# Performance work log

Measured on AMD Instinct MI355X. Metric: run time of the kernel, lower is better.

## Reference

```python
import jax, jax.numpy as jnp
import numpy as np

VOCAB, NUM_LABELS, EMB, H = 50000, 5, 512, 1024
B, S = 32, 256


def setup_inputs() -> dict:
    key = jax.random.key(0)
    ks = jax.random.split(key, 7)
    tokens = jax.random.randint(ks[0], (B, S), 0, VOCAB)
    scale_e = 0.05
    emb = jax.random.normal(ks[1], (VOCAB, EMB), dtype=jnp.float32) * scale_e
    # Keras LSTM kernels: input kernel [EMB,4H], recurrent kernel [H,4H], bias [4H]
    W = jax.random.normal(ks[2], (EMB, 4 * H), dtype=jnp.float32) / np.sqrt(EMB)
    U = jax.random.normal(ks[3], (H, 4 * H), dtype=jnp.float32) / np.sqrt(H)
    # unit_forget_bias=True: forget-gate bias block initialized to 1
    b = jnp.concatenate([
        jnp.zeros((H,), jnp.float32),
        jnp.ones((H,), jnp.float32),
        jnp.zeros((2 * H,), jnp.float32),
    ])
    Wd = jax.random.normal(ks[4], (H, NUM_LABELS), dtype=jnp.float32) / np.sqrt(H)
    bd = jnp.zeros((NUM_LABELS,), jnp.float32)
    return {"tokens": tokens, "emb": emb, "W": W, "U": U, "b": b, "Wd": Wd, "bd": bd}


def _lstm_last_h(x, W, U, b):
    # x: [B,S,EMB] -> last hidden state [B,H]
    xt = jnp.swapaxes(x, 0, 1)  # [S,B,EMB]
    # precompute input projections for all steps: [S,B,4H]
    xz = jnp.einsum('sbe,eg->sbg', xt, W) + b
    h0 = jnp.zeros((x.shape[0], H), x.dtype)
    c0 = jnp.zeros((x.shape[0], H), x.dtype)

    def step(carry, xz_t):
        h, c = carry
        z = xz_t + h @ U  # [B,4H]
        i, f, g, o = jnp.split(z, 4, axis=-1)  # Keras gate order i,f,c,o
        i = jax.nn.sigmoid(i)
        f = jax.nn.sigmoid(f)
        g = jnp.tanh(g)
        o = jax.nn.sigmoid(o)
        c = f * c + i * g
        h = o * jnp.tanh(c)
        return (h, c), None

    (h_last, _), _ = jax.lax.scan(step, (h0, c0), xz)
    return h_last


def reference(tokens, emb, W, U, b, Wd, bd):
    x = emb[tokens]  # [B,S,EMB] embedding lookup
    h = _lstm_last_h(x, W, U, b)  # [B,H]
    logits = h @ Wd + bd  # [B,NUM_LABELS]
    return logits
```

## Files before the change

kernel.cpp:

```cpp
#include <hip/hip_runtime.h>
#include <hip/hip_fp16.h>

#define B_   32
#define S_   256
#define EMB_ 512
#define H_   1024
#define G4_  4096
#define NL_  5
#define NBLK 128

typedef _Float16 f16x8 __attribute__((ext_vector_type(8)));
typedef float f32x4 __attribute__((ext_vector_type(4)));
typedef unsigned long long ull;

__device__ inline ull ldq(const ull* p) {
  return __hip_atomic_load(p, __ATOMIC_RELAXED, __HIP_MEMORY_SCOPE_AGENT);
}
__device__ inline unsigned ldw(const unsigned* p) {
  return __hip_atomic_load(p, __ATOMIC_RELAXED, __HIP_MEMORY_SCOPE_AGENT);
}
__device__ inline void stw(unsigned* p, unsigned v) {
  __hip_atomic_store(p, v, __ATOMIC_RELAXED, __HIP_MEMORY_SCOPE_AGENT);
}

__global__ __launch_bounds__(256) void k_transposeK(const float* __restrict__ src,
                                                    float* __restrict__ dst, int K) {
  __shared__ float tile[32][33];
  int c0 = blockIdx.x * 32, k0 = blockIdx.y * 32;
  int tx = threadIdx.x & 31, ty = threadIdx.x >> 5;
#pragma unroll
  for (int i = 0; i < 4; ++i)
    tile[ty + 8 * i][tx] = src[(size_t)(k0 + ty + 8 * i) * G4_ + c0 + tx];
  __syncthreads();
#pragma unroll
  for (int i = 0; i < 4; ++i)
    dst[(size_t)(c0 + ty + 8 * i) * K + k0 + tx] = tile[tx][ty + 8 * i];
}

__global__ __launch_bounds__(256) void k_prepU16(const float* __restrict__ Ut,
                                                 f16x8* __restrict__ Ubf) {
  int gid = blockIdx.x * 256 + threadIdx.x;
  int l = gid & 63;
  int bxws = gid >> 6;
  int n = l & 15, kgrp = l >> 4;
  int s = bxws & 7, bw = bxws >> 3;
  int w = bw & 3, bx = bw >> 2;
  int g = n & 3, ju = n >> 2;
  int gcol = g * 1024 + bx * 4 + ju;
  int kbase = w * 256 + s * 32 + kgrp * 8;
  const float4* f = (const float4*)(Ut + (size_t)gcol * H_ + kbase);
  float4 f0 = f[0], f1 = f[1];
  float v[8] = {f0.x, f0.y, f0.z, f0.w, f1.x, f1.y, f1.z, f1.w};
  f16x8 vh, vl;
#pragma unroll
  for (int j = 0; j < 8; ++j) {
    _Float16 hi = (_Float16)v[j];
    vh[j] = hi;
    vl[j] = (_Float16)((v[j] - (float)hi) * 1024.f);
  }
  Ubf[(size_t)bxws * 128 + l] = vh;
  Ubf[(size_t)bxws * 128 + 64 + l] = vl;
}

__global__ __launch_bounds__(256) void k_prepW16(const float* __restrict__ Wt,
                                                 unsigned short* __restrict__ Wf16) {
  int gid = blockIdx.x * 256 + threadIdx.x;
  int l = gid & 63, fi = gid >> 6;
  int kc = fi & 15, ug = fi >> 4;
  int n16 = l & 15, kgrp = l >> 4;
  int gcol = (n16 & 3) * 1024 + ug * 4 + (n16 >> 2);
  const float4* f = (const float4*)(Wt + (size_t)gcol * 512 + kc * 32 + kgrp * 8);
  float4 f0 = f[0], f1 = f[1];
  float v[8] = {f0.x, f0.y, f0.z, f0.w, f1.x, f1.y, f1.z, f1.w};
  union { unsigned short u[8]; uint4 q; } o;
#pragma unroll
  for (int j = 0; j < 8; ++j) o.u[j] = __half_as_ushort(__float2half_rn(v[j]));
  *(uint4*)(Wf16 + ((size_t)fi * 64 + l) * 8) = o.q;
}

__global__ __launch_bounds__(256) void k_prepX(const int* __restrict__ tokens,
                                               const float* __restrict__ emb,
                                               unsigned short* __restrict__ Xf16) {
  int gid = blockIdx.x * 256 + threadIdx.x;
  int seg = gid & 63, row = gid >> 6;
  int s = row >> 5, b = row & 31;
  int tok = tokens[b * 256 + s];
  const float4* f = (const float4*)(emb + (size_t)tok * EMB_ + seg * 8);
  float4 f0 = f[0], f1 = f[1];
  float v[8] = {f0.x, f0.y, f0.z, f0.w, f1.x, f1.y, f1.z, f1.w};
  union { unsigned short u[8]; uint4 q; } o;
#pragma unroll
  for (int j = 0; j < 8; ++j) o.u[j] = __half_as_ushort(__float2half_rn(v[j]));
  *(uint4*)(Xf16 + (size_t)row * 512 + seg * 8) = o.q;
}

__global__ __launch_bounds__(512, 2) void k_steps11(
    const f16x8* __restrict__ Ubf,
    const unsigned short* __restrict__ Wf16,
    const unsigned short* __restrict__ Xf16,
    const float* __restrict__ bias,
    unsigned* __restrict__ T0, unsigned* __restrict__ T1,
    unsigned* __restrict__ flg) {
  __shared__ f16x8 UL[8192];
  __shared__ float red[4096];

  const int tid = threadIdx.x;
  const int bx = blockIdx.x;
  const int l = tid & 63, w = tid >> 6;

#pragma unroll
  for (int i = 0; i < 16; ++i) {
    int flat = i * 512 + tid;
    int ll = flat & 63, s8 = (flat >> 6) & 7, ks = (flat >> 9) & 3;
    int pl = (flat >> 11) & 1, cg = flat >> 12;
    size_t fi = (size_t)((bx * 2 + cg) * 4 + ks) * 8 + s8;
    UL[flat] = Ubf[fi * 128 + pl * 64 + ll];
  }

  const int gb = tid & 31, gu = tid >> 5;
  const int gm2 = gb >> 4, gcg = gu >> 2, gju = gu & 3;
  const int gle = ((gb & 15) >> 2) * 16 + gju * 4;
  const int grr = gb & 3;
  const int widx = (((gb >> 4) * 128 + bx) * 16 + (gb & 15)) * 4 + (gu >> 1);
  float bia[4];
#pragma unroll
  for (int g = 0; g < 4; ++g) bia[g] = bias[g * 1024 + bx * 8 + gu];
  float creg = 0.f;

  const int ks_w = w >> 1;
  const int xrow0 = (l & 15) * 512 + (l >> 4) * 8;
  const unsigned* myflg = flg + (size_t)((w * 16 + (l >> 2)) * 4 + (l & 3)) * 16;

  __syncthreads();

  for (int t = 0; t < S_; ++t) {
    const ull* R64 = (const ull*)((t & 1) ? T0 : T1);
    unsigned* WrT = (t & 1) ? T1 : T0;

    f32x4 acc[2][2], accL[2][2];
#pragma unroll
    for (int cg = 0; cg < 2; ++cg)
#pragma unroll
      for (int m2 = 0; m2 < 2; ++m2) {
        acc[cg][m2] = (f32x4){0.f, 0.f, 0.f, 0.f};
        accL[cg][m2] = (f32x4){0.f, 0.f, 0.f, 0.f};
      }
    {
      const unsigned short* Xt = Xf16 + (size_t)t * 16384;
#pragma unroll
      for (int c2 = 0; c2 < 2; ++c2) {
        int kc = w * 2 + c2;
        f16x8 xa0 = *(const f16x8*)(Xt + xrow0 + kc * 32);
        f16x8 xa1 = *(const f16x8*)(Xt + 8192 + xrow0 + kc * 32);
        f16x8 wb0 = *(const f16x8*)(Wf16 + ((size_t)((bx * 2 + 0) * 16 + kc) * 64 + l) * 8);
        f16x8 wb1 = *(const f16x8*)(Wf16 + ((size_t)((bx * 2 + 1) * 16 + kc) * 64 + l) * 8);
        acc[0][0] = __builtin_amdgcn_mfma_f32_16x16x32_f16(xa0, wb0, acc[0][0], 0, 0, 0);
        acc[0][1] = __builtin_amdgcn_mfma_f32_16x16x32_f16(xa1, wb0, acc[0][1], 0, 0, 0);
        acc[1][0] = __builtin_amdgcn_mfma_f32_16x16x32_f16(xa0, wb1, acc[1][0], 0, 0, 0);
        acc[1][1] = __builtin_amdgcn_mfma_f32_16x16x32_f16(xa1, wb1, acc[1][1], 0, 0, 0);
      }
    }

    if (t > 0) {
      const unsigned tg = (unsigned)t;
      while (true) {
        unsigned v = ldw(myflg);
        if (__all((int)(v >= tg))) break;
        __builtin_amdgcn_s_sleep(1);
      }
      union F { ull q[2]; f16x8 v; };
      F A[2][4];
#pragma unroll
      for (int m2 = 0; m2 < 2; ++m2)
#pragma unroll
        for (int s = 0; s < 4; ++s) {
          int kidx = w * 16 + s * 4 + (l >> 4);
          int b64 = ((m2 * 128 + kidx) * 16 + (l & 15)) * 2;
          A[m2][s].q[0] = ldq(R64 + b64);
          A[m2][s].q[1] = ldq(R64 + b64 + 1);
        }
#pragma unroll
      for (int s = 0; s < 4; ++s) {
        int s8 = (w & 1) * 4 + s;
#pragma unroll
        for (int cg = 0; cg < 2; ++cg) {
          f16x8 uhf = UL[cg * 4096 + ks_w * 512 + s8 * 64 + l];
          f16x8 ulf = UL[cg * 4096 + 2048 + ks_w * 512 + s8 * 64 + l];
          acc[cg][0]  = __builtin_amdgcn_mfma_f32_16x16x32_f16(A[0][s].v, uhf, acc[cg][0], 0, 0, 0);
          acc[cg][1]  = __builtin_amdgcn_mfma_f32_16x16x32_f16(A[1][s].v, uhf, acc[cg][1], 0, 0, 0);
          accL[cg][0] = __builtin_amdgcn_mfma_f32_16x16x32_f16(A[0][s].v, ulf, accL[cg][0], 0, 0, 0);
          accL[cg][1] = __builtin_amdgcn_mfma_f32_16x16x32_f16(A[1][s].v, ulf, accL[cg][1], 0, 0, 0);
        }
      }
    }

#pragma unroll
    for (int cg = 0; cg < 2; ++cg)
#pragma unroll
      for (int m2 = 0; m2 < 2; ++m2)
        acc[cg][m2] += accL[cg][m2] * 9.765625e-4f;

    if (w < 4) {
#pragma unroll
      for (int cg = 0; cg < 2; ++cg) {
        *(f32x4*)(&red[((w * 2 + 0) * 2 + cg) * 256 + l * 4]) = acc[cg][0];
        *(f32x4*)(&red[((w * 2 + 1) * 2 + cg) * 256 + l * 4]) = acc[cg][1];
      }
    }
    __syncthreads();
    if (w >= 4) {
      int w4 = w - 4;
#pragma unroll
      for (int cg = 0; cg < 2; ++cg) {
        f32x4* p0 = (f32x4*)(&red[((w4 * 2 + 0) * 2 + cg) * 256 + l * 4]);
        f32x4* p1 = (f32x4*)(&red[((w4 * 2 + 1) * 2 + cg) * 256 + l * 4]);
        *p0 += acc[cg][0];
        *p1 += acc[cg][1];
      }
    }
    __syncthreads();

    if (tid < 256) {
      float z[4];
#pragma unroll
      for (int g = 0; g < 4; ++g) z[g] = bia[g];
#pragma unroll
      for (int w4 = 0; w4 < 4; ++w4) {
        int sb = ((w4 * 2 + gm2) * 2 + gcg) * 256;
#pragma unroll
        for (int g = 0; g < 4; ++g)
          z[g] += red[sb + (gle + g) * 4 + grr];
      }
      float ig = 1.f / (1.f + __expf(-z[0]));
      float fg = 1.f / (1.f + __expf(-z[1]));
      float gg = tanhf(z[2]);
      float og = 1.f / (1.f + __expf(-z[3]));
      creg = fg * creg + ig * gg;
      float hv = og * tanhf(creg);
      unsigned pk = (unsigned)__half_as_ushort(__float2half_rn(hv));
      unsigned other = (unsigned)__shfl_xor((int)pk, 32, 64);
      if ((gu & 1) == 0)
        stw(WrT + widx, (pk & 0xffffu) | (other << 16));
      asm volatile("s_waitcnt vmcnt(0)" ::: "memory");
      if ((tid & 63) == 0)
        stw(flg + (size_t)(bx * 4 + (tid >> 6)) * 16, (unsigned)(t + 1));
    }
    __syncthreads();
  }
}

__global__ __launch_bounds__(256) void k_head6(const unsigned* __restrict__ T,
                                               const float* __restrict__ Wd,
                                               const float* __restrict__ bd,
                                               float* __restrict__ out) {
  __shared__ float red[32 * 9];
  int lbl = blockIdx.x;
  int tid = threadIdx.x;
  int b = tid >> 3, ks = tid & 7;
  float acc = 0.f;
  for (int k = ks * 128; k < ks * 128 + 128; ++k) {
    int idx = (((b >> 4) * 128 + (k >> 3)) * 16 + (b & 15)) * 4 + ((k & 7) >> 1);
    unsigned wv = T[idx];
    unsigned short h16 = (unsigned short)((k & 1) ? (wv >> 16) : (wv & 0xffffu));
    acc += __half2float(__ushort_as_half(h16)) * Wd[k * NL_ + lbl];
  }
  red[b * 9 + ks] = acc;
  __syncthreads();
  if (tid < 32) {
    float s = bd[lbl];
#pragma unroll
    for (int i = 0; i < 8; ++i) s += red[tid * 9 + i];
    out[tid * NL_ + lbl] = s;
  }
}

extern "C" void kernel_launch(void* const* d_in, const int* in_sizes, int n_in,
                              void* d_out, int out_size, void* d_ws, size_t ws_size,
                              hipStream_t stream) {
  const int* tokens  = (const int*)d_in[0];
  const float* emb   = (const float*)d_in[1];
  const float* W     = (const float*)d_in[2];
  const float* U     = (const float*)d_in[3];
  const float* bias  = (const float*)d_in[4];
  const float* Wd    = (const float*)d_in[5];
  const float* bd    = (const float*)d_in[6];
  float* out = (float*)d_out;

  char* ws = (char*)d_ws;
  unsigned short* Xf16 = (unsigned short*)ws;
  unsigned short* Wf16 = (unsigned short*)(ws + 8388608);
  float* Ut          = (float*)(ws + 16777216);
  float* Wt          = (float*)(ws + 33554432);
  f16x8* Ubf         = (f16x8*)(ws + 41943040);
  unsigned* T0       = (unsigned*)(ws + 58720256);
  unsigned* T1       = (unsigned*)(ws + 58785792);
  unsigned* flg      = (unsigned*)(ws + 58851328);

  hipMemsetAsync(flg, 0, 32768, stream);
  k_transposeK<<<dim3(128, 32), 256, 0, stream>>>(U, Ut, 1024);
  k_prepU16<<<2048, 256, 0, stream>>>(Ut, Ubf);
  k_transposeK<<<dim3(128, 16), 256, 0, stream>>>(W, Wt, 512);
  k_prepW16<<<1024, 256, 0, stream>>>(Wt, Wf16);
  k_prepX<<<2048, 256, 0, stream>>>(tokens, emb, Xf16);

  k_steps11<<<NBLK, 512, 0, stream>>>(Ubf, Wf16, Xf16, bias, T0, T1, flg);

  k_head6<<<NL_, 256, 0, stream>>>(T1, Wd, bd, out);
}
```

Baseline: 1.139 ms.

## Double-buffer gate reduction, drop a barrier, stream low U half from global

Restructures the per-step reduction in the persistent LSTM kernel. All 8 waves now write partials into a double-buffered LDS array and all 512 threads reduce them into a gate buffer, which removes one of the three barriers per step. The low-precision half of U is re-read from global/L2 each step instead of living in LDS, halving the U footprint in shared memory. Sigmoid and tanh are replaced with fast rcp/exp forms, which costs some accuracy and risks overflow in the exp-based tanh for large inputs.

```diff
diff --git a/kernel.cpp b/kernel.cpp
--- a/kernel.cpp
+++ b/kernel.cpp
@@ -21,6 +21,13 @@
 }
 __device__ inline void stw(unsigned* p, unsigned v) {
   __hip_atomic_store(p, v, __ATOMIC_RELAXED, __HIP_MEMORY_SCOPE_AGENT);
+}
+__device__ inline float sigm(float x) {
+  return __builtin_amdgcn_rcpf(1.f + __expf(-x));
+}
+__device__ inline float ftanh(float x) {
+  float e = __expf(2.f * x);
+  return (e - 1.f) * __builtin_amdgcn_rcpf(e + 1.f);
 }
 
 __global__ __launch_bounds__(256) void k_transposeK(const float* __restrict__ src,
@@ -94,37 +101,42 @@
   *(uint4*)(Xf16 + (size_t)row * 512 + seg * 8) = o.q;
 }
 
-__global__ __launch_bounds__(512, 2) void k_steps11(
+__global__ __launch_bounds__(512, 2) void k_steps12(
     const f16x8* __restrict__ Ubf,
     const unsigned short* __restrict__ Wf16,
     const unsigned short* __restrict__ Xf16,
     const float* __restrict__ bias,
     unsigned* __restrict__ T0, unsigned* __restrict__ T1,
     unsigned* __restrict__ flg) {
-  __shared__ f16x8 UL[8192];
-  __shared__ float red[4096];
+  __shared__ f16x8 UL[4096];
+  __shared__ float red[2][8192];
+  __shared__ float zg[2][1056];
+  __shared__ float bias_s[32];
 
   const int tid = threadIdx.x;
   const int bx = blockIdx.x;
   const int l = tid & 63, w = tid >> 6;
 
 #pragma unroll
-  for (int i = 0; i < 16; ++i) {
+  for (int i = 0; i < 8; ++i) {
     int flat = i * 512 + tid;
     int ll = flat & 63, s8 = (flat >> 6) & 7, ks = (flat >> 9) & 3;
-    int pl = (flat >> 11) & 1, cg = flat >> 12;
+    int cg = flat >> 11;
     size_t fi = (size_t)((bx * 2 + cg) * 4 + ks) * 8 + s8;
-    UL[flat] = Ubf[fi * 128 + pl * 64 + ll];
-  }
+    UL[flat] = Ubf[fi * 128 + ll];
+  }
+  if (tid < 32) {
+    int cg = tid >> 4, n16 = tid & 15;
+    bias_s[tid] = bias[(n16 & 3) * 1024 + (bx * 2 + cg) * 4 + (n16 >> 2)];
+  }
+
+  const int e = tid & 255, m = tid >> 8;
+  const int n16r = (e >> 2) & 15;
+  const int zb = m * 16 + (e >> 6) * 4 + (e & 3);
 
   const int gb = tid & 31, gu = tid >> 5;
-  const int gm2 = gb >> 4, gcg = gu >> 2, gju = gu & 3;
-  const int gle = ((gb & 15) >> 2) * 16 + gju * 4;
-  const int grr = gb & 3;
   const int widx = (((gb >> 4) * 128 + bx) * 16 + (gb & 15)) * 4 + (gu >> 1);
-  float bia[4];
-#pragma unroll
-  for (int g = 0; g < 4; ++g) bia[g] = bias[g * 1024 + bx * 8 + gu];
+  const int zrd = gb * 33 + (gu >> 2) * 16 + (gu & 3) * 4;
   float creg = 0.f;
 
   const int ks_w = w >> 1;
@@ -134,8 +146,17 @@
   __syncthreads();
 
   for (int t = 0; t < S_; ++t) {
-    const ull* R64 = (const ull*)((t & 1) ? T0 : T1);
-    unsigned* WrT = (t & 1) ? T1 : T0;
+    const int par = t & 1;
+    const ull* R64 = (const ull*)(par ? T0 : T1);
+    unsigned* WrT = par ? T1 : T0;
+
+    f16x8 ulo[4][2];
+#pragma unroll
+    for (int s = 0; s < 4; ++s)
+#pragma unroll
+      for (int cg = 0; cg < 2; ++cg)
+        ulo[s][cg] = Ubf[((size_t)((bx * 2 + cg) * 4 + ks_w) * 8 +
+                          (w & 1) * 4 + s) * 128 + 64 + l];
 
     f32x4 acc[2][2], accL[2][2];
 #pragma unroll
@@ -184,12 +205,11 @@
         int s8 = (w & 1) * 4 + s;
 #pragma unroll
         for (int cg = 0; cg < 2; ++cg) {
-          f16x8 uhf = UL[cg * 4096 + ks_w * 512 + s8 * 64 + l];
-          f16x8 ulf = UL[cg * 4096 + 2048 + ks_w * 512 + s8 * 64 + l];
+          f16x8 uhf = UL[cg * 2048 + ks_w * 512 + s8 * 64 + l];
           acc[cg][0]  = __builtin_amdgcn_mfma_f32_16x16x32_f16(A[0][s].v, uhf, acc[cg][0], 0, 0, 0);
           acc[cg][1]  = __builtin_amdgcn_mfma_f32_16x16x32_f16(A[1][s].v, uhf, acc[cg][1], 0, 0, 0);
-          accL[cg][0] = __builtin_amdgcn_mfma_f32_16x16x32_f16(A[0][s].v, ulf, accL[cg][0], 0, 0, 0);
-          accL[cg][1] = __builtin_amdgcn_mfma_f32_16x16x32_f16(A[1][s].v, ulf, accL[cg][1], 0, 0, 0);
+          accL[cg][0] = __builtin_amdgcn_mfma_f32_16x16x32_f16(A[0][s].v, ulo[s][cg], accL[cg][0], 0, 0, 0);
+          accL[cg][1] = __builtin_amdgcn_mfma_f32_16x16x32_f16(A[1][s].v, ulo[s][cg], accL[cg][1], 0, 0, 0);
         }
       }
     }
@@ -200,43 +220,36 @@
       for (int m2 = 0; m2 < 2; ++m2)
         acc[cg][m2] += accL[cg][m2] * 9.765625e-4f;
 
-    if (w < 4) {
-#pragma unroll
-      for (int cg = 0; cg < 2; ++cg) {
-        *(f32x4*)(&red[((w * 2 + 0) * 2 + cg) * 256 + l * 4]) = acc[cg][0];
-        *(f32x4*)(&red[((w * 2 + 1) * 2 + cg) * 256 + l * 4]) = acc[cg][1];
-      }
+#pragma unroll
+    for (int cg = 0; cg < 2; ++cg)
+#pragma unroll
+      for (int m2 = 0; m2 < 2; ++m2)
+        *(f32x4*)(&red[par][(w * 4 + m2 * 2 + cg) * 256 + l * 4]) = acc[cg][m2];
+    __syncthreads();
+
+    {
+      float z0 = bias_s[n16r], z1 = bias_s[16 + n16r];
+#pragma unroll
+      for (int ww = 0; ww < 8; ++ww) {
+        z0 += red[par][(ww * 4 + m * 2 + 0) * 256 + e];
+        z1 += red[par][(ww * 4 + m * 2 + 1) * 256 + e];
+      }
+      zg[par][zb * 33 + n16r] = z0;
+      zg[par][zb * 33 + 16 + n16r] = z1;
     }
     __syncthreads();
-    if (w >= 4) {
-      int w4 = w - 4;
-#pragma unroll
-      for (int cg = 0; cg < 2; ++cg) {
-        f32x4* p0 = (f32x4*)(&red[((w4 * 2 + 0) * 2 + cg) * 256 + l * 4]);
-        f32x4* p1 = (f32x4*)(&red[((w4 * 2 + 1) * 2 + cg) * 256 + l * 4]);
-        *p0 += acc[cg][0];
-        *p1 += acc[cg][1];
-      }
-    }
-    __syncthreads();
 
     if (tid < 256) {
-      float z[4];
-#pragma unroll
-      for (int g = 0; g < 4; ++g) z[g] = bia[g];
-#pragma unroll
-      for (int w4 = 0; w4 < 4; ++w4) {
-        int sb = ((w4 * 2 + gm2) * 2 + gcg) * 256;
-#pragma unroll
-        for (int g = 0; g < 4; ++g)
-          z[g] += red[sb + (gle + g) * 4 + grr];
-      }
-      float ig = 1.f / (1.f + __expf(-z[0]));
-      float fg = 1.f / (1.f + __expf(-z[1]));
-      float gg = tanhf(z[2]);
-      float og = 1.f / (1.f + __expf(-z[3]));
+      float zi = zg[par][zrd + 0];
+      float zf = zg[par][zrd + 1];
+      float zc = zg[par][zrd + 2];
+      float zo = zg[par][zrd + 3];
+      float ig = sigm(zi);
+      float fg = sigm(zf);
+      float gg = ftanh(zc);
+      float og = sigm(zo);
       creg = fg * creg + ig * gg;
-      float hv = og * tanhf(creg);
+      float hv = og * ftanh(creg);
       unsigned pk = (unsigned)__half_as_ushort(__float2half_rn(hv));
       unsigned other = (unsigned)__shfl_xor((int)pk, 32, 64);
       if ((gu & 1) == 0)
@@ -245,7 +258,6 @@
       if ((tid & 63) == 0)
         stw(flg + (size_t)(bx * 4 + (tid >> 6)) * 16, (unsigned)(t + 1));
     }
-    __syncthreads();
   }
 }
 
@@ -303,7 +315,7 @@
   k_prepW16<<<1024, 256, 0, stream>>>(Wt, Wf16);
   k_prepX<<<2048, 256, 0, stream>>>(tokens, emb, Xf16);
 
-  k_steps11<<<NBLK, 512, 0, stream>>>(Ubf, Wf16, Xf16, bias, T0, T1, flg);
+  k_steps12<<<NBLK, 512, 0, stream>>>(Ubf, Wf16, Xf16, bias, T0, T1, flg);
 
   k_head6<<<NL_, 256, 0, stream>>>(T1, Wd, bd, out);
 }
```

Measured after the change: 1.039 ms (median of 2 runs). -8.8%, faster.
